# Kernel optimization log

Hardware: AMD Instinct MI355X
Metric: run time of the kernel (lower is better)

## Reference

```python
import jax, jax.numpy as jnp
import numpy as np

B, T, U, V = 8, 128, 64, 1024
BLANK = V - 1  # blank=-1 resolves to last class index


def setup_inputs() -> dict:
    key = jax.random.key(0)
    k1, k2, k3, k4 = jax.random.split(key, 4)
    logits = jax.random.normal(k1, (B, T, U + 1, V), dtype=jnp.float32)
    targets = jax.random.randint(k2, (B, U), 0, V - 1, dtype=jnp.int32)  # exclude blank
    logit_lengths = jax.random.randint(k3, (B,), T // 2, T + 1, dtype=jnp.int32)
    target_lengths = jax.random.randint(k4, (B,), U // 2, U + 1, dtype=jnp.int32)
    return {
        "logits": logits,
        "targets": targets,
        "logit_lengths": logit_lengths,
        "target_lengths": target_lengths,
    }


def _rnnt_neglogp(logits, targets, logit_lengths, target_lengths, blank):
    """RNNT forward-variable DP (Graves 2012). Returns per-sample -log p(y|x)."""
    Bn, Tn, U1, Vn = logits.shape
    Un = U1 - 1
    lp = jax.nn.log_softmax(logits, axis=-1)  # fused_log_softmax=True
    lp_blank = lp[..., blank]                                  # (B, T, U+1)
    idx = jnp.broadcast_to(targets[:, None, :, None], (Bn, Tn, Un, 1))
    lp_emit = jnp.take_along_axis(lp[:, :, :Un, :], idx, axis=-1)[..., 0]  # (B, T, U)

    # alpha[t, u]: log-prob of emitting first u labels using first t frames.
    # alpha[0, u] = sum_{v<u} emit(0, v)
    row0 = jnp.concatenate(
        [jnp.zeros((Bn, 1), lp.dtype), jnp.cumsum(lp_emit[:, 0, :], axis=-1)], axis=1
    )  # (B, U+1)

    def inner(a_prev, x):
        # a[u] = logaddexp(alpha[t-1,u] + blank(t-1,u),  a[u-1] + emit(t,u-1))
        b_u, e_u = x
        a_new = jnp.logaddexp(b_u, a_prev + e_u)
        return a_new, a_new

    def outer(prev_row, x):
        blank_prev, emit_t = x  # (B, U+1), (B, U)
        b_term = prev_row + blank_prev  # vertical (blank) transition term
        _, rest = jax.lax.scan(
            inner, b_term[:, 0], (b_term[:, 1:].T, emit_t.T)
        )  # rest: (U, B)
        new_row = jnp.concatenate([b_term[:, :1], rest.T], axis=1)  # (B, U+1)
        return new_row, new_row

    xs = (
        jnp.swapaxes(lp_blank[:, :-1, :], 0, 1),  # (T-1, B, U+1)
        jnp.swapaxes(lp_emit[:, 1:, :], 0, 1),    # (T-1, B, U)
    )
    _, rows = jax.lax.scan(outer, row0, xs)
    alpha = jnp.concatenate([row0[None], rows], axis=0)  # (T, B, U+1)

    bidx = jnp.arange(Bn)
    t_last = logit_lengths - 1
    u_last = target_lengths
    a_end = alpha[t_last, bidx, u_last]
    final_blank = lp_blank[bidx, t_last, u_last]
    return -(a_end + final_blank)


def reference(logits, targets, logit_lengths, target_lengths):
    return _rnnt_neglogp(logits, targets, logit_lengths, target_lengths, BLANK)
```

## Files before the change

### kernel.cpp

```cpp
#include <hip/hip_runtime.h>
#include <hip/hip_bf16.h>

#define BB 8
#define TT 128
#define UU 64
#define VV 1024
#define U1 65
#define NROWS (BB * TT * U1)
#define DSZ ((TT + UU) * U1)

__device__ __forceinline__ float wave_max64(float v) {
#pragma unroll
    for (int off = 32; off; off >>= 1) v = fmaxf(v, __shfl_xor(v, off, 64));
    return v;
}
__device__ __forceinline__ float wave_sum64(float v) {
#pragma unroll
    for (int off = 32; off; off >>= 1) v += __shfl_xor(v, off, 64);
    return v;
}

__global__ __launch_bounds__(256) void rnnt_lse_kernel(
    const float* __restrict__ logits, const int* __restrict__ targets,
    float* __restrict__ bdiag, float* __restrict__ ediag) {
    const int wave = threadIdx.x >> 6;
    const int lane = threadIdx.x & 63;
    const int row  = blockIdx.x * 4 + wave;
    const float* rowp = logits + (size_t)row * VV;
    const float4* p4 = (const float4*)rowp;

    float4 x0 = p4[lane];
    float4 x1 = p4[lane + 64];
    float4 x2 = p4[lane + 128];
    float4 x3 = p4[lane + 192];

    float m = fmaxf(fmaxf(fmaxf(x0.x, x0.y), fmaxf(x0.z, x0.w)),
                    fmaxf(fmaxf(x1.x, x1.y), fmaxf(x1.z, x1.w)));
    m = fmaxf(m, fmaxf(fmaxf(fmaxf(x2.x, x2.y), fmaxf(x2.z, x2.w)),
                       fmaxf(fmaxf(x3.x, x3.y), fmaxf(x3.z, x3.w))));
    m = wave_max64(m);

    float s = __expf(x0.x - m) + __expf(x0.y - m) + __expf(x0.z - m) + __expf(x0.w - m)
            + __expf(x1.x - m) + __expf(x1.y - m) + __expf(x1.z - m) + __expf(x1.w - m)
            + __expf(x2.x - m) + __expf(x2.y - m) + __expf(x2.z - m) + __expf(x2.w - m)
            + __expf(x3.x - m) + __expf(x3.y - m) + __expf(x3.z - m) + __expf(x3.w - m);
    s = wave_sum64(s);

    if (lane == 0) {
        float lse = m + __logf(s);
        int b   = row / (TT * U1);
        int rem = row - b * (TT * U1);
        int t   = rem / U1;
        int u   = rem - t * U1;
        int dpos = (t + u) * U1 + u;
        bdiag[b * DSZ + dpos] = rowp[VV - 1] - lse;
        if (u < UU) {
            int tgt = targets[b * UU + u];
            ediag[b * DSZ + dpos] = rowp[tgt] - lse;
        }
    }
}

__global__ __launch_bounds__(128) void rnnt_dp_kernel(
    const float* __restrict__ bdiag, const float* __restrict__ ediag,
    const int* __restrict__ logit_lengths, const int* __restrict__ target_lengths,
    float* __restrict__ out) {
    const int b = blockIdx.x;
    const int u = threadIdx.x;
    const float* gb = bdiag + b * DSZ;
    const float* ge = ediag + b * DSZ;
    const int tl = logit_lengths[b] - 1;
    const int ul = target_lengths[b];

    __shared__ float buf0[U1], buf1[U1];
    __shared__ float s_res;
    float* prev = buf0;
    float* cur  = buf1;

    const bool lane_ok = (u <= UU);
    float bd_n = lane_ok ? gb[u] : 0.f;
    float ed_n = (lane_ok && u >= 1) ? ge[u - 1] : 0.f;

    if (u == 0) cur[0] = 0.f;
    __syncthreads();
    { float* tmp = prev; prev = cur; cur = tmp; }

    for (int d = 1; d < TT + UU; ++d) {
        float bd = bd_n, ed = ed_n;
        if (d < TT + UU - 1) {
            bd_n = lane_ok ? gb[d * U1 + u] : 0.f;
            ed_n = (lane_ok && u >= 1) ? ge[d * U1 + u - 1] : 0.f;
        }
        const int t = d - u;
        if (lane_ok && t >= 0 && t < TT) {
            const float NEG = -1e30f;
            float va = (t >= 1) ? prev[u]     + bd : NEG;
            float vb = (u >= 1) ? prev[u - 1] + ed : NEG;
            float mm = fmaxf(va, vb);
            float r  = mm + __logf(__expf(va - mm) + __expf(vb - mm));
            cur[u] = r;
            if (t == tl && u == ul) s_res = r;
        }
        __syncthreads();
        { float* tmp = prev; prev = cur; cur = tmp; }
    }

    if (u == 0) out[b] = -(s_res + gb[(tl + ul) * U1 + ul]);
}

extern "C" void kernel_launch(void* const* d_in, const int* in_sizes, int n_in,
                              void* d_out, int out_size, void* d_ws, size_t ws_size,
                              hipStream_t stream) {
    const float* logits         = (const float*)d_in[0];
    const int*   targets        = (const int*)d_in[1];
    const int*   logit_lengths  = (const int*)d_in[2];
    const int*   target_lengths = (const int*)d_in[3];
    float* outp = (float*)d_out;

    float* bdiag = (float*)d_ws;
    float* ediag = bdiag + (size_t)BB * DSZ;

    rnnt_lse_kernel<<<NROWS / 4, 256, 0, stream>>>(logits, targets, bdiag, ediag);
    rnnt_dp_kernel<<<BB, 128, 0, stream>>>(bdiag, ediag, logit_lengths,
                                           target_lengths, outp);
}
```

Baseline: 457.5 us.

## Run RNNT DP in a single wave with shuffles and chunked LDS staging

The DP kernel now uses one 64-lane wave per batch item. Neighbour alpha values pass through __shfl_up instead of shared memory and __syncthreads, and the 65th column is computed redundantly in every lane. Blank and emit log-probs are packed as float2 per diagonal, and chunks of 48 diagonals are double-buffered into LDS through registers. The LSE kernel now gets the blank and target logits by wave shuffle from values already in registers, avoiding extra global reads. This removes per-step block barriers and global latency from the serial DP, but adds a large register array for prefetch and redundant column-64 work.

```diff
diff --git a/kernel.cpp b/kernel.cpp
--- a/kernel.cpp
+++ b/kernel.cpp
@@ -7,7 +7,10 @@
 #define VV 1024
 #define U1 65
 #define NROWS (BB * TT * U1)
-#define DSZ ((TT + UU) * U1)
+#define NDIAG (TT + UU)
+#define DSZ (NDIAG * U1)
+#define CD 48
+#define CH_F4 ((CD * U1) / 2)
 
 __device__ __forceinline__ float wave_max64(float v) {
 #pragma unroll
@@ -22,12 +25,11 @@
 
 __global__ __launch_bounds__(256) void rnnt_lse_kernel(
     const float* __restrict__ logits, const int* __restrict__ targets,
-    float* __restrict__ bdiag, float* __restrict__ ediag) {
+    float2* __restrict__ P) {
     const int wave = threadIdx.x >> 6;
     const int lane = threadIdx.x & 63;
     const int row  = blockIdx.x * 4 + wave;
-    const float* rowp = logits + (size_t)row * VV;
-    const float4* p4 = (const float4*)rowp;
+    const float4* p4 = (const float4*)(logits + (size_t)row * VV);
 
     float4 x0 = p4[lane];
     float4 x1 = p4[lane + 64];
@@ -45,67 +47,100 @@
             + __expf(x2.x - m) + __expf(x2.y - m) + __expf(x2.z - m) + __expf(x2.w - m)
             + __expf(x3.x - m) + __expf(x3.y - m) + __expf(x3.z - m) + __expf(x3.w - m);
     s = wave_sum64(s);
+    const float lse = m + __logf(s);
 
-    if (lane == 0) {
-        float lse = m + __logf(s);
-        int b   = row / (TT * U1);
-        int rem = row - b * (TT * U1);
-        int t   = rem / U1;
-        int u   = rem - t * U1;
-        int dpos = (t + u) * U1 + u;
-        bdiag[b * DSZ + dpos] = rowp[VV - 1] - lse;
-        if (u < UU) {
-            int tgt = targets[b * UU + u];
-            ediag[b * DSZ + dpos] = rowp[tgt] - lse;
-        }
+    const int b   = row / (TT * U1);
+    const int rem = row - b * (TT * U1);
+    const int t   = rem / U1;
+    const int u   = rem - t * U1;
+
+    const float blankv = __shfl(x3.w, 63, 64) - lse;
+    float emitv = 0.f;
+    if (u < UU) {
+        const int tgt = targets[b * UU + u];
+        const int q = tgt >> 2, grp = q >> 6, sl = q & 63, c = tgt & 3;
+        float4 g4 = (grp == 0) ? x0 : (grp == 1) ? x1 : (grp == 2) ? x2 : x3;
+        float cv = (c == 0) ? g4.x : (c == 1) ? g4.y : (c == 2) ? g4.z : g4.w;
+        emitv = __shfl(cv, sl, 64) - lse;
     }
+    if (lane == 0) P[(size_t)b * DSZ + (t + u) * U1 + u] = make_float2(blankv, emitv);
 }
 
-__global__ __launch_bounds__(128) void rnnt_dp_kernel(
-    const float* __restrict__ bdiag, const float* __restrict__ ediag,
-    const int* __restrict__ logit_lengths, const int* __restrict__ target_lengths,
-    float* __restrict__ out) {
+__global__ __launch_bounds__(64) void rnnt_dp_kernel(
+    const float2* __restrict__ P, const int* __restrict__ logit_lengths,
+    const int* __restrict__ target_lengths, float* __restrict__ out) {
     const int b = blockIdx.x;
-    const int u = threadIdx.x;
-    const float* gb = bdiag + b * DSZ;
-    const float* ge = ediag + b * DSZ;
+    const int l = threadIdx.x;
+    const float2* Pg = P + (size_t)b * DSZ;
     const int tl = logit_lengths[b] - 1;
     const int ul = target_lengths[b];
 
-    __shared__ float buf0[U1], buf1[U1];
-    __shared__ float s_res;
-    float* prev = buf0;
-    float* cur  = buf1;
+    __shared__ __align__(16) float2 sb[2][CD * U1];
 
-    const bool lane_ok = (u <= UU);
-    float bd_n = lane_ok ? gb[u] : 0.f;
-    float ed_n = (lane_ok && u >= 1) ? ge[u - 1] : 0.f;
+    const float NEG = -1e30f;
+    float aprev   = (l == 0) ? 0.f : NEG;
+    float aprev64 = NEG;
+    float res = 0.f;
 
-    if (u == 0) cur[0] = 0.f;
-    __syncthreads();
-    { float* tmp = prev; prev = cur; cur = tmp; }
+    {
+        const float4* g4 = (const float4*)Pg;
+#pragma unroll
+        for (int i = 0; i < 25; ++i) {
+            int idx = i * 64 + l;
+            if (idx < CH_F4) ((float4*)sb[0])[idx] = g4[idx];
+        }
+    }
 
-    for (int d = 1; d < TT + UU; ++d) {
-        float bd = bd_n, ed = ed_n;
-        if (d < TT + UU - 1) {
-            bd_n = lane_ok ? gb[d * U1 + u] : 0.f;
-            ed_n = (lane_ok && u >= 1) ? ge[d * U1 + u - 1] : 0.f;
+    int d = 1;
+    for (int g = 0; g < 4; ++g) {
+        float4 v[25];
+        if (g < 3) {
+            const float4* g4 = (const float4*)Pg + (size_t)(g + 1) * CH_F4;
+#pragma unroll
+            for (int i = 0; i < 25; ++i) {
+                int idx = i * 64 + l;
+                if (idx < CH_F4) v[i] = g4[idx];
+            }
         }
-        const int t = d - u;
-        if (lane_ok && t >= 0 && t < TT) {
-            const float NEG = -1e30f;
-            float va = (t >= 1) ? prev[u]     + bd : NEG;
-            float vb = (u >= 1) ? prev[u - 1] + ed : NEG;
+        const float2* buf = sb[g & 1];
+#pragma unroll 1
+        for (int i = 0; i < CD; ++i, ++d) {
+            const int c = g * CD + i;
+            if (c > NDIAG - 2) break;
+            float2 pr  = buf[i * U1 + l];
+            float2 p64 = buf[i * U1 + 64];
+            float edl = __shfl_up(pr.y, 1, 64);
+            float al  = __shfl_up(aprev, 1, 64);
+            const int t = d - l;
+            float va = (t >= 1) ? aprev + pr.x : NEG;
+            float vb = (l >= 1) ? al + edl : NEG;
             float mm = fmaxf(va, vb);
             float r  = mm + __logf(__expf(va - mm) + __expf(vb - mm));
-            cur[u] = r;
-            if (t == tl && u == ul) s_res = r;
+            r = (t >= 0 && t < TT) ? r : NEG;
+            const int t64 = d - 64;
+            float va64 = (t64 >= 1) ? aprev64 + p64.x : NEG;
+            float vb64 = aprev + pr.y;
+            float mm64 = fmaxf(va64, vb64);
+            float r64  = mm64 + __logf(__expf(va64 - mm64) + __expf(vb64 - mm64));
+            r64 = (t64 >= 0) ? r64 : NEG;
+            if (d == tl + ul) {
+                if (ul < 64) { if (l == ul) res = r; }
+                else if (l == 63) res = r64;
+            }
+            aprev = r; aprev64 = r64;
         }
-        __syncthreads();
-        { float* tmp = prev; prev = cur; cur = tmp; }
+        if (g < 3) {
+            float4* dst = (float4*)sb[(g + 1) & 1];
+#pragma unroll
+            for (int i = 0; i < 25; ++i) {
+                int idx = i * 64 + l;
+                if (idx < CH_F4) dst[idx] = v[i];
+            }
+        }
     }
 
-    if (u == 0) out[b] = -(s_res + gb[(tl + ul) * U1 + ul]);
+    const float rr = __shfl(res, (ul < 64) ? ul : 63, 64);
+    if (l == 0) out[b] = -(rr + Pg[(tl + ul) * U1 + ul].x);
 }
 
 extern "C" void kernel_launch(void* const* d_in, const int* in_sizes, int n_in,
@@ -117,10 +152,8 @@
     const int*   target_lengths = (const int*)d_in[3];
     float* outp = (float*)d_out;
 
-    float* bdiag = (float*)d_ws;
-    float* ediag = bdiag + (size_t)BB * DSZ;
+    float2* P = (float2*)d_ws;
 
-    rnnt_lse_kernel<<<NROWS / 4, 256, 0, stream>>>(logits, targets, bdiag, ediag);
-    rnnt_dp_kernel<<<BB, 128, 0, stream>>>(bdiag, ediag, logit_lengths,
-                                           target_lengths, outp);
+    rnnt_lse_kernel<<<NROWS / 4, 256, 0, stream>>>(logits, targets, P);
+    rnnt_dp_kernel<<<BB, 64, 0, stream>>>(P, logit_lengths, target_lengths, outp);
 }
```

New measurement: 434.7 us. -5.0%, faster.
